# Kernel tuning notes

Hardware: AMD Instinct MI355X
Metric: run time of the kernel (lower is better)

The kernel has to match this reference:

```python
import jax, jax.numpy as jnp
import numpy as np

B, T, F, H = 1024, 256, 23, 100  # batch, timesteps, lab features, LSTM hidden
S_IN, S_OUT = 6, 20              # fc_state: Linear(6, 20)
FC_IN, N_CLS = 120, 2            # fc: Linear(120, 2)


def setup_inputs() -> dict:
    key = jax.random.key(0)
    ks = jax.random.split(key, 10)
    sc = 0.1  # weight init scale
    return {
        "x_lab": jax.random.normal(ks[0], (B, T, F), jnp.float32),
        "t_lab": jax.random.uniform(ks[1], (1, B, T), jnp.float32, minval=0.0, maxval=10.0),
        "x_state": jax.random.normal(ks[2], (B, S_IN), jnp.float32),
        # time-aware LSTM (LSTM2) params
        "W_x": jax.random.normal(ks[3], (F, 4 * H), jnp.float32) * sc,
        "W_h": jax.random.normal(ks[4], (H, 4 * H), jnp.float32) * sc,
        "b_lstm": jnp.zeros((4 * H,), jnp.float32),
        "W_d": jax.random.normal(ks[5], (H, H), jnp.float32) * sc,   # cell-decomposition weight
        "b_d": jnp.zeros((H,), jnp.float32),
        # fc_state: Linear(6, 20)
        "W_state": jax.random.normal(ks[6], (S_IN, S_OUT), jnp.float32) * sc,
        "b_state": jnp.zeros((S_OUT,), jnp.float32),
        # fc: Linear(120, 2)
        "W_fc": jax.random.normal(ks[7], (FC_IN, N_CLS), jnp.float32) * sc,
        "b_fc": jnp.zeros((N_CLS,), jnp.float32),
    }


def reference(x_lab, t_lab, x_state, W_x, W_h, b_lstm, W_d, b_d,
              W_state, b_state, W_fc, b_fc):
    # Time-aware LSTM (T-LSTM style): decompose prev cell into short-term
    # memory, decay it by g(dt) = 1 / log(e + dt), then standard LSTM gates.
    dt = jnp.transpose(t_lab[0])            # [T, B] elapsed-time deltas
    xs = jnp.transpose(x_lab, (1, 0, 2))    # [T, B, F]
    # Precompute input projections for all steps (one big GEMM).
    x_proj = jnp.einsum('tbf,fg->tbg', xs, W_x) + b_lstm  # [T, B, 4H]

    def step(carry, inp):
        h, c = carry                          # [B, H] each
        xp, d = inp                           # [B, 4H], [B]
        c_short = jnp.tanh(c @ W_d + b_d)     # short-term memory
        decay = (1.0 / jnp.log(jnp.e + d))[:, None]
        c_adj = c - c_short + c_short * decay # long-term + decayed short-term
        gates = xp + h @ W_h                  # [B, 4H]
        i, f, g, o = jnp.split(gates, 4, axis=1)
        i = jax.nn.sigmoid(i)
        f = jax.nn.sigmoid(f)
        o = jax.nn.sigmoid(o)
        g = jnp.tanh(g)
        c_new = f * c_adj + i * g
        h_new = o * jnp.tanh(c_new)
        return (h_new, c_new), None

    b = x_lab.shape[0]
    init = (jnp.zeros((b, H), x_lab.dtype), jnp.zeros((b, H), x_lab.dtype))
    (h_final, _), _ = jax.lax.scan(step, init, (x_proj, dt))

    e_state = x_state @ W_state + b_state          # [B, 20]
    y = jnp.concatenate([h_final, e_state], axis=1) @ W_fc + b_fc  # [B, 2]
    return jax.nn.softmax(y, axis=1)
```

## Files before the change

kernel.cpp:

```cpp
#include <hip/hip_runtime.h>

#define TT   256
#define FF   23
#define HH   100
#define NROW 4
#define NTHR 512
#define NWG  256

typedef unsigned int  u32;
typedef unsigned short u16;
typedef __attribute__((ext_vector_type(8))) short short8;
typedef __attribute__((ext_vector_type(4))) float f32x4;

__device__ __forceinline__ u16 f2bf(float f){
  u32 u = __float_as_uint(f);
  u += 0x7fffu + ((u >> 16) & 1u);
  return (u16)(u >> 16);
}
__device__ __forceinline__ float fsig(float x){
  return __builtin_amdgcn_rcpf(1.0f + __expf(-x));
}
__device__ __forceinline__ float ftanh(float x){
  return 1.0f - 2.0f * __builtin_amdgcn_rcpf(__expf(2.0f * x) + 1.0f);
}


__global__ __launch_bounds__(NTHR, 2) void tlstm4(
    const float* __restrict__ x_lab,  const float* __restrict__ t_lab,
    const float* __restrict__ x_state,const float* __restrict__ W_x,
    const float* __restrict__ W_h,    const float* __restrict__ b_lstm,
    const float* __restrict__ W_d,    const float* __restrict__ b_d,
    const float* __restrict__ W_state,const float* __restrict__ b_state,
    const float* __restrict__ W_fc,   const float* __restrict__ b_fc,
    float* __restrict__ out)
{
  __shared__ __align__(16) short sHC[2][2][512];
  __shared__ __align__(16) short sX[2][128];
  __shared__ __align__(16) float sDec[TT * NROW];
  __shared__ __align__(16) float sHF[NROW][128];

  const int tid  = threadIdx.x;
  const int lane = tid & 63;
  const int w    = tid >> 6;
  const int nl   = lane & 15;
  const int q4   = lane >> 4;
  const int b0   = blockIdx.x * NROW;
  const int j    = w * 16 + nl;
  const bool jr  = (j < HH);

  for (int i = tid; i < 2*2*512; i += NTHR) ((short*)sHC)[i] = 0;
  for (int i = tid; i < 2*128;   i += NTHR) ((short*)sX)[i]  = 0;

  for (int e = tid; e < TT*NROW; e += NTHR) {
    int t = e >> 2, r = e & 3;
    sDec[e] = 1.0f / logf(2.718281828459045f + t_lab[(b0 + r)*TT + t]);
  }
  if (tid < NROW*FF) {
    int r = tid / FF, f = tid % FF;
    sX[0][r*32 + f] = (short)f2bf(x_lab[((b0 + r)*TT + 0)*FF + f]);
  }

  short8 wh[4][3], wd[4], wx[4];
#pragma unroll
  for (int g = 0; g < 4; ++g)
#pragma unroll
    for (int kf = 0; kf < 3; ++kf) {
      short8 v;
#pragma unroll
      for (int i = 0; i < 8; ++i) {
        int k = kf*32 + q4*8 + i;
        v[i] = (short)(jr ? f2bf(W_h[k*400 + g*HH + j]) : 0);
      }
      wh[g][kf] = v;
    }
#pragma unroll
  for (int kf = 0; kf < 4; ++kf) {
    short8 v;
#pragma unroll
    for (int i = 0; i < 8; ++i) {
      int k = kf*32 + q4*8 + i;
      v[i] = (short)((k < HH && jr) ? f2bf(W_d[k*HH + j]) : 0);
    }
    wd[kf] = v;
  }
#pragma unroll
  for (int g = 0; g < 4; ++g) {
    short8 v;
#pragma unroll
    for (int i = 0; i < 8; ++i) {
      int k = q4*8 + i;
      float x = 0.f;
      if (jr) {
        if (k < FF)                 x = W_x[k*400 + g*HH + j];
        else if (k >= 24 && k < 28) x = W_h[(96 + (k-24))*400 + g*HH + j];
      }
      v[i] = (short)f2bf(x);
    }
    wx[g] = v;
  }

  float bl[4], bd;
#pragma unroll
  for (int g = 0; g < 4; ++g) bl[g] = jr ? b_lstm[g*HH + j] : 0.f;
  bd = jr ? b_d[j] : 0.f;

  __syncthreads();

  const bool rdr  = ((nl & 3) == 0);
  const int rbase = (nl >> 2)*32 + q4*8;
  const int widx  = (j >> 5)*128 + q4*32 + ((j >> 3) & 3)*8 + (j & 7);

  short8 ha[3] = {}, ca[4] = {}, xa = {};
  float cm = 0.f;
  float hl = 0.f;

  for (int t = 0; t < TT; ++t) {
    if (w < 7) {
      const short* hb = sHC[t & 1][0];
      const short* cb = sHC[t & 1][1];
      if (rdr) {
#pragma unroll
        for (int kf = 0; kf < 3; ++kf) ha[kf] = *(const short8*)(hb + kf*128 + rbase);
#pragma unroll
        for (int kf = 0; kf < 4; ++kf) ca[kf] = *(const short8*)(cb + kf*128 + rbase);
        xa = *(const short8*)(sX[t & 1] + rbase);
      }
      float dec = sDec[t*4 + q4];

      f32x4 accD = {bd, bd, bd, bd};
#pragma unroll
      for (int kf = 0; kf < 4; ++kf)
        accD = __builtin_amdgcn_mfma_f32_16x16x32_bf16(ca[kf], wd[kf], accD, 0, 0, 0);

      f32x4 acc[4];
#pragma unroll
      for (int g = 0; g < 4; ++g) {
        f32x4 a = {bl[g], bl[g], bl[g], bl[g]};
        a = __builtin_amdgcn_mfma_f32_16x16x32_bf16(xa, wx[g], a, 0, 0, 0);
#pragma unroll
        for (int kf = 0; kf < 3; ++kf)
          a = __builtin_amdgcn_mfma_f32_16x16x32_bf16(ha[kf], wh[g][kf], a, 0, 0, 0);
        acc[g] = a;
      }

      float cs   = ftanh(accD[0]);
      float cadj = cm - cs + cs*dec;
      float ig = fsig(acc[0][0]);
      float fg = fsig(acc[1][0]);
      float gg = ftanh(acc[2][0]);
      float og = fsig(acc[3][0]);
      float cnv = fg*cadj + ig*gg;
      cm = cnv;
      float hv = og*ftanh(cnv);
      hl = hv;

      short* hn = sHC[(t + 1) & 1][0];
      short* cn = sHC[(t + 1) & 1][1];
      hn[widx] = (short)f2bf(hv);
      cn[widx] = (short)f2bf(cnv);
      if (w == 6 && nl < 4)
        sX[(t + 1) & 1][q4*32 + 24 + nl] = (short)f2bf(hv);
    } else {
      if (t + 1 < TT) {
        int e0 = lane;
        if (e0 < NROW*FF) {
          int pr = e0 / FF, pf = e0 % FF;
          sX[(t + 1) & 1][pr*32 + pf] =
              (short)f2bf(x_lab[((b0 + pr)*TT + (t + 1))*FF + pf]);
        }
        int e1 = lane + 64;
        if (e1 < NROW*FF) {
          int pr = e1 / FF, pf = e1 % FF;
          sX[(t + 1) & 1][pr*32 + pf] =
              (short)f2bf(x_lab[((b0 + pr)*TT + (t + 1))*FF + pf]);
        }
      }
    }
    __syncthreads();
  }

  if (w < 7) sHF[q4][j] = hl;
  __syncthreads();

  if (tid < NROW) {
    const int bg = b0 + tid;
    float y0 = b_fc[0], y1 = b_fc[1];
    for (int k = 0; k < HH; ++k) {
      float hv = sHF[tid][k];
      y0 += hv * W_fc[2*k];
      y1 += hv * W_fc[2*k + 1];
    }
#pragma unroll
    for (int k = 0; k < 20; ++k) {
      float a = b_state[k];
#pragma unroll
      for (int s = 0; s < 6; ++s) a += x_state[bg*6 + s] * W_state[s*20 + k];
      y0 += a * W_fc[2*(HH + k)];
      y1 += a * W_fc[2*(HH + k) + 1];
    }
    float m = fmaxf(y0, y1);
    float e0 = __expf(y0 - m), e1 = __expf(y1 - m);
    float inv = 1.0f / (e0 + e1);
    out[bg*2 + 0] = e0 * inv;
    out[bg*2 + 1] = e1 * inv;
  }
}

extern "C" void kernel_launch(void* const* d_in, const int* in_sizes, int n_in,
                              void* d_out, int out_size, void* d_ws, size_t ws_size,
                              hipStream_t stream) {
  const float* x_lab   = (const float*)d_in[0];
  const float* t_lab   = (const float*)d_in[1];
  const float* x_state = (const float*)d_in[2];
  const float* W_x     = (const float*)d_in[3];
  const float* W_h     = (const float*)d_in[4];
  const float* b_lstm  = (const float*)d_in[5];
  const float* W_d     = (const float*)d_in[6];
  const float* b_d     = (const float*)d_in[7];
  const float* W_state = (const float*)d_in[8];
  const float* b_state = (const float*)d_in[9];
  const float* W_fc    = (const float*)d_in[10];
  const float* b_fc    = (const float*)d_in[11];
  float* outp = (float*)d_out;

  hipLaunchKernelGGL(tlstm4, dim3(NWG), dim3(NTHR), 0, stream,
                     x_lab, t_lab, x_state, W_x, W_h, b_lstm, W_d, b_d,
                     W_state, b_state, W_fc, b_fc, outp);
}
```

Baseline: 186.5 us.

## Preload all timestep inputs into LDS, drop loader wave, split MFMA chains

Before the recurrence, each workgroup converts its entire x_lab slice to bf16 and stores it in a shared-memory buffer of 256x128 shorts (64 KB). This removes the dedicated eighth wave that prefetched x from global memory every step, so the block shrinks to 7 waves. The per-step MFMA accumulation is also split into two independent accumulator chains for both the gates and the decomposition, which shortens the dependent MFMA latency chain. The cost is far more LDS per block (about 64 KB extra), which may limit occupancy to fewer blocks per CU, plus an upfront load phase that is not overlapped with compute.

```diff
diff --git a/kernel.cpp b/kernel.cpp
--- a/kernel.cpp
+++ b/kernel.cpp
@@ -4,7 +4,7 @@
 #define FF   23
 #define HH   100
 #define NROW 4
-#define NTHR 512
+#define NTHR 448
 #define NWG  256
 
 typedef unsigned int  u32;
@@ -25,7 +25,7 @@
 }
 
 
-__global__ __launch_bounds__(NTHR, 2) void tlstm4(
+__global__ __launch_bounds__(NTHR, 2) void tlstm5(
     const float* __restrict__ x_lab,  const float* __restrict__ t_lab,
     const float* __restrict__ x_state,const float* __restrict__ W_x,
     const float* __restrict__ W_h,    const float* __restrict__ b_lstm,
@@ -34,8 +34,8 @@
     const float* __restrict__ W_fc,   const float* __restrict__ b_fc,
     float* __restrict__ out)
 {
+  __shared__ __align__(16) short sXall[TT * 128];
   __shared__ __align__(16) short sHC[2][2][512];
-  __shared__ __align__(16) short sX[2][128];
   __shared__ __align__(16) float sDec[TT * NROW];
   __shared__ __align__(16) float sHF[NROW][128];
 
@@ -48,16 +48,16 @@
   const int j    = w * 16 + nl;
   const bool jr  = (j < HH);
 
-  for (int i = tid; i < 2*2*512; i += NTHR) ((short*)sHC)[i] = 0;
-  for (int i = tid; i < 2*128;   i += NTHR) ((short*)sX)[i]  = 0;
-
-  for (int e = tid; e < TT*NROW; e += NTHR) {
+  for (int i = tid; i < 1024; i += NTHR) ((u32*)sHC)[i] = 0u;
+
+  for (int e = tid; e < TT * 128; e += NTHR) {
+    int t = e >> 7, inner = e & 127, r = inner >> 5, f = inner & 31;
+    float x = (f < FF) ? x_lab[((b0 + r)*TT + t)*FF + f] : 0.f;
+    sXall[e] = (short)f2bf(x);
+  }
+  for (int e = tid; e < TT * NROW; e += NTHR) {
     int t = e >> 2, r = e & 3;
     sDec[e] = 1.0f / logf(2.718281828459045f + t_lab[(b0 + r)*TT + t]);
-  }
-  if (tid < NROW*FF) {
-    int r = tid / FF, f = tid % FF;
-    sX[0][r*32 + f] = (short)f2bf(x_lab[((b0 + r)*TT + 0)*FF + f]);
   }
 
   short8 wh[4][3], wd[4], wx[4];
@@ -114,72 +114,60 @@
   float cm = 0.f;
   float hl = 0.f;
 
+  const f32x4 zv = {0.f, 0.f, 0.f, 0.f};
+
   for (int t = 0; t < TT; ++t) {
-    if (w < 7) {
-      const short* hb = sHC[t & 1][0];
-      const short* cb = sHC[t & 1][1];
-      if (rdr) {
-#pragma unroll
-        for (int kf = 0; kf < 3; ++kf) ha[kf] = *(const short8*)(hb + kf*128 + rbase);
-#pragma unroll
-        for (int kf = 0; kf < 4; ++kf) ca[kf] = *(const short8*)(cb + kf*128 + rbase);
-        xa = *(const short8*)(sX[t & 1] + rbase);
-      }
-      float dec = sDec[t*4 + q4];
-
-      f32x4 accD = {bd, bd, bd, bd};
-#pragma unroll
-      for (int kf = 0; kf < 4; ++kf)
-        accD = __builtin_amdgcn_mfma_f32_16x16x32_bf16(ca[kf], wd[kf], accD, 0, 0, 0);
-
-      f32x4 acc[4];
-#pragma unroll
-      for (int g = 0; g < 4; ++g) {
-        f32x4 a = {bl[g], bl[g], bl[g], bl[g]};
-        a = __builtin_amdgcn_mfma_f32_16x16x32_bf16(xa, wx[g], a, 0, 0, 0);
-#pragma unroll
-        for (int kf = 0; kf < 3; ++kf)
-          a = __builtin_amdgcn_mfma_f32_16x16x32_bf16(ha[kf], wh[g][kf], a, 0, 0, 0);
-        acc[g] = a;
-      }
-
-      float cs   = ftanh(accD[0]);
-      float cadj = cm - cs + cs*dec;
-      float ig = fsig(acc[0][0]);
-      float fg = fsig(acc[1][0]);
-      float gg = ftanh(acc[2][0]);
-      float og = fsig(acc[3][0]);
-      float cnv = fg*cadj + ig*gg;
-      cm = cnv;
-      float hv = og*ftanh(cnv);
-      hl = hv;
-
-      short* hn = sHC[(t + 1) & 1][0];
-      short* cn = sHC[(t + 1) & 1][1];
-      hn[widx] = (short)f2bf(hv);
-      cn[widx] = (short)f2bf(cnv);
-      if (w == 6 && nl < 4)
-        sX[(t + 1) & 1][q4*32 + 24 + nl] = (short)f2bf(hv);
-    } else {
-      if (t + 1 < TT) {
-        int e0 = lane;
-        if (e0 < NROW*FF) {
-          int pr = e0 / FF, pf = e0 % FF;
-          sX[(t + 1) & 1][pr*32 + pf] =
-              (short)f2bf(x_lab[((b0 + pr)*TT + (t + 1))*FF + pf]);
-        }
-        int e1 = lane + 64;
-        if (e1 < NROW*FF) {
-          int pr = e1 / FF, pf = e1 % FF;
-          sX[(t + 1) & 1][pr*32 + pf] =
-              (short)f2bf(x_lab[((b0 + pr)*TT + (t + 1))*FF + pf]);
-        }
-      }
-    }
+    const short* hb = sHC[t & 1][0];
+    const short* cb = sHC[t & 1][1];
+    if (rdr) {
+      xa = *(const short8*)(sXall + t*128 + rbase);
+#pragma unroll
+      for (int kf = 0; kf < 4; ++kf) ca[kf] = *(const short8*)(cb + kf*128 + rbase);
+#pragma unroll
+      for (int kf = 0; kf < 3; ++kf) ha[kf] = *(const short8*)(hb + kf*128 + rbase);
+    }
+    float dec = sDec[t*4 + q4];
+
+    f32x4 a0[4], a1[4];
+#pragma unroll
+    for (int g = 0; g < 4; ++g) {
+      f32x4 b = {bl[g], bl[g], bl[g], bl[g]};
+      a0[g] = __builtin_amdgcn_mfma_f32_16x16x32_bf16(xa, wx[g], b, 0, 0, 0);
+    }
+    f32x4 d0 = {bd, bd, bd, bd}, d1 = zv;
+    d0 = __builtin_amdgcn_mfma_f32_16x16x32_bf16(ca[0], wd[0], d0, 0, 0, 0);
+    d1 = __builtin_amdgcn_mfma_f32_16x16x32_bf16(ca[1], wd[1], d1, 0, 0, 0);
+    d0 = __builtin_amdgcn_mfma_f32_16x16x32_bf16(ca[2], wd[2], d0, 0, 0, 0);
+    d1 = __builtin_amdgcn_mfma_f32_16x16x32_bf16(ca[3], wd[3], d1, 0, 0, 0);
+#pragma unroll
+    for (int g = 0; g < 4; ++g) {
+      a1[g] = __builtin_amdgcn_mfma_f32_16x16x32_bf16(ha[0], wh[g][0], zv,    0, 0, 0);
+      a0[g] = __builtin_amdgcn_mfma_f32_16x16x32_bf16(ha[1], wh[g][1], a0[g], 0, 0, 0);
+      a1[g] = __builtin_amdgcn_mfma_f32_16x16x32_bf16(ha[2], wh[g][2], a1[g], 0, 0, 0);
+    }
+
+    float cs   = ftanh(d0[0] + d1[0]);
+    float cadj = cm - cs + cs*dec;
+    float ig = fsig (a0[0][0] + a1[0][0]);
+    float fg = fsig (a0[1][0] + a1[1][0]);
+    float gg = ftanh(a0[2][0] + a1[2][0]);
+    float og = fsig (a0[3][0] + a1[3][0]);
+    float cnv = fg*cadj + ig*gg;
+    cm = cnv;
+    float hv = og*ftanh(cnv);
+    hl = hv;
+
+    short* hn = sHC[(t + 1) & 1][0];
+    short* cn = sHC[(t + 1) & 1][1];
+    hn[widx] = (short)f2bf(hv);
+    cn[widx] = (short)f2bf(cnv);
+    if (w == 6 && nl < 4 && t + 1 < TT)
+      sXall[(t + 1)*128 + q4*32 + 24 + nl] = (short)f2bf(hv);
+
     __syncthreads();
   }
 
-  if (w < 7) sHF[q4][j] = hl;
+  sHF[q4][j] = hl;
   __syncthreads();
 
   if (tid < NROW) {
@@ -223,7 +211,7 @@
   const float* b_fc    = (const float*)d_in[11];
   float* outp = (float*)d_out;
 
-  hipLaunchKernelGGL(tlstm4, dim3(NWG), dim3(NTHR), 0, stream,
+  hipLaunchKernelGGL(tlstm5, dim3(NWG), dim3(NTHR), 0, stream,
                      x_lab, t_lab, x_state, W_x, W_h, b_lstm, W_d, b_d,
                      W_state, b_state, W_fc, b_fc, outp);
 }
```

Result: slower. 196.0 us (+5.1%).
